# Optimization experiments

Measured on AMD Instinct MI355X. Metric: run time of the kernel, lower is better.

## Reference

```python
import jax, jax.numpy as jnp
import numpy as np

B, L, D = 4, 512, 128

def setup_inputs() -> dict:
    key = jax.random.key(0)
    k1, k2, k3, k4 = jax.random.split(key, 4)
    s = 1.0 / np.sqrt(D)
    return {
        "inp": jax.random.normal(k1, (B, L, D), dtype=jnp.float32),
        "Wu": jax.random.normal(k2, (D, D), dtype=jnp.float32) * s,
        "Ww": jax.random.normal(k3, (D, D), dtype=jnp.float32) * s,
        "Wv": jax.random.normal(k4, (1, D), dtype=jnp.float32) * s,
    }

def reference(inp, Wu, Ww, Wv):
    # inp: (B,L,D); torch Linear weights are (out,in), so y = x @ W.T
    qu = inp @ Wu.T                      # (B,L,D), u(inp)
    kw = inp @ Ww.T                      # (B,L,D), w(inp)
    # qu.unsqueeze(1) -> broadcast over i; kw.unsqueeze(2) -> broadcast over j
    # h[b,i,j,:] = tanh(u(inp)[b,j] + w(inp)[b,i])   (dropout = identity in eval)
    h = jnp.tanh(qu[:, None, :, :] + kw[:, :, None, :])   # (B,L,L,D)
    score = jnp.einsum('bijd,d->bij', h, Wv[0])           # (B,L,L)
    attn = jax.nn.softmax(score, axis=2)                  # softmax over keys j
    out = jnp.einsum('bij,bjd->bid', attn, inp)           # bmm(attn, inp)
    return out, attn
```

## Files before the change

### kernel.cpp

```cpp
#include <hip/hip_runtime.h>

#define BD 128
#define SL 512
#define NB 4

__device__ __forceinline__ float rcp_fast(float x) { return __builtin_amdgcn_rcpf(x); }

__global__ __launch_bounds__(256) void k_tr(const float* __restrict__ Wu,
                                            const float* __restrict__ Ww,
                                            float* __restrict__ WuT,
                                            float* __restrict__ WwT) {
    int idx = blockIdx.x * 256 + threadIdx.x;
    int k = idx >> 7, o = idx & 127;
    WuT[idx] = Wu[o * BD + k];
    WwT[idx] = Ww[o * BD + k];
}

__global__ __launch_bounds__(256) void k_qk(const float* __restrict__ inp,
                                            const float* __restrict__ WuT,
                                            const float* __restrict__ WwT,
                                            float* __restrict__ Equ2,
                                            float* __restrict__ Ekw) {
    __shared__ float sx[2][BD];
    const int t = threadIdx.x, m = t >> 7, o = t & 127;
    const int blk = blockIdx.x;
    const int x   = blk & 7;
    const int b   = x >> 1;
    const int rp  = (blk >> 3) * 2 + (x & 1);
    const int r0  = b * SL + rp * 2;
    const int l0  = rp * 2;
    const int jp  = l0 >> 1;

    sx[t >> 7][t & 127] = inp[(size_t)r0 * BD + t];
    __syncthreads();

    const float* WT = m ? WwT : WuT;
    float acc0 = 0.f, acc1 = 0.f;
    #pragma unroll 4
    for (int k = 0; k < BD; k += 4) {
        float w0 = WT[(k + 0) * BD + o];
        float w1 = WT[(k + 1) * BD + o];
        float w2 = WT[(k + 2) * BD + o];
        float w3 = WT[(k + 3) * BD + o];
        float4 x0 = *(const float4*)&sx[0][k];
        float4 x1 = *(const float4*)&sx[1][k];
        acc0 = fmaf(x0.x, w0, acc0); acc0 = fmaf(x0.y, w1, acc0);
        acc0 = fmaf(x0.z, w2, acc0); acc0 = fmaf(x0.w, w3, acc0);
        acc1 = fmaf(x1.x, w0, acc1); acc1 = fmaf(x1.y, w1, acc1);
        acc1 = fmaf(x1.z, w2, acc1); acc1 = fmaf(x1.w, w3, acc1);
    }

    if (m == 0) {
        size_t base = (((size_t)b * 32 + (o >> 2)) * 256 + jp) * 8 + (o & 3);
        Equ2[base]     = __expf(2.f * acc0);
        Equ2[base + 4] = __expf(2.f * acc1);
    } else {
        Ekw[(size_t)(r0 + 0) * BD + o] = __expf(2.f * acc0);
        Ekw[(size_t)(r0 + 1) * BD + o] = __expf(2.f * acc1);
    }
}

__global__ __launch_bounds__(1024, 8) void k_attn(const float* __restrict__ inp,
                                                  const float* __restrict__ Wv,
                                                  const float* __restrict__ Equ2,
                                                  const float* __restrict__ Ekw,
                                                  float* __restrict__ out,
                                                  float* __restrict__ attn) {
    __shared__ float  s_pT[SL * 4];
    __shared__ float  s_ap[8192];
    __shared__ float4 s_E[BD];
    __shared__ float  s_u[BD];
    __shared__ float  s_rB[4 * 8];

    const int t   = threadIdx.x;
    const int blk = blockIdx.x;
    const int x   = blk & 7;
    const int b   = x >> 1;
    const int it  = (blk >> 3) * 2 + (x & 1);
    const int i0  = it * 4;

    if (t < BD) {
        const float* ek = Ekw + ((size_t)b * SL + i0) * BD + t;
        float u = rcp_fast(Wv[t]);
        s_E[t] = make_float4(ek[0] * u, ek[BD] * u, ek[2 * BD] * u, ek[3 * BD] * u);
        s_u[t] = u;
    }
    __syncthreads();

    const int jp = t & 255, dg = t >> 8;
    const float4* equ4 = (const float4*)(Equ2 + (size_t)b * BD * SL);
    float a0[4] = {0.f, 0.f, 0.f, 0.f};
    float a1[4] = {0.f, 0.f, 0.f, 0.f};
    #pragma unroll 2
    for (int cc = 0; cc < 8; ++cc) {
        int c = dg * 8 + cc;
        float4 qA = equ4[(c * 256 + jp) * 2 + 0];
        float4 qB = equ4[(c * 256 + jp) * 2 + 1];
        float4 E0 = s_E[c * 4 + 0];
        float4 E1 = s_E[c * 4 + 1];
        float4 E2 = s_E[c * 4 + 2];
        float4 E3 = s_E[c * 4 + 3];
        float4 uu = *(const float4*)&s_u[c * 4];
        float e0[4] = {E0.x, E0.y, E0.z, E0.w};
        float e1[4] = {E1.x, E1.y, E1.z, E1.w};
        float e2[4] = {E2.x, E2.y, E2.z, E2.w};
        float e3[4] = {E3.x, E3.y, E3.z, E3.w};
        #pragma unroll
        for (int i = 0; i < 4; ++i) {
            float xa0 = fmaf(qA.x, e0[i], uu.x);
            float xa1 = fmaf(qA.y, e1[i], uu.y);
            a0[i] = fmaf(xa0 + xa1, rcp_fast(xa0 * xa1), a0[i]);
            float xa2 = fmaf(qA.z, e2[i], uu.z);
            float xa3 = fmaf(qA.w, e3[i], uu.w);
            a0[i] = fmaf(xa2 + xa3, rcp_fast(xa2 * xa3), a0[i]);
            float xb0 = fmaf(qB.x, e0[i], uu.x);
            float xb1 = fmaf(qB.y, e1[i], uu.y);
            a1[i] = fmaf(xb0 + xb1, rcp_fast(xb0 * xb1), a1[i]);
            float xb2 = fmaf(qB.z, e2[i], uu.z);
            float xb3 = fmaf(qB.w, e3[i], uu.w);
            a1[i] = fmaf(xb2 + xb3, rcp_fast(xb2 * xb3), a1[i]);
        }
    }
    #pragma unroll
    for (int i = 0; i < 4; ++i) {
        s_ap[((dg * 2 + 0) * 4 + i) * 256 + jp] = a0[i];
        s_ap[((dg * 2 + 1) * 4 + i) * 256 + jp] = a1[i];
    }
    __syncthreads();

    const int j = t & 511, dh = t >> 9, ro = dh * 2;
    const int jpp = j >> 1, jj = j & 1, w8 = j >> 6;
    float af[2];
    #pragma unroll
    for (int ii = 0; ii < 2; ++ii) {
        int r = ro + ii;
        af[ii] = s_ap[((0 * 2 + jj) * 4 + r) * 256 + jpp]
               + s_ap[((1 * 2 + jj) * 4 + r) * 256 + jpp]
               + s_ap[((2 * 2 + jj) * 4 + r) * 256 + jpp]
               + s_ap[((3 * 2 + jj) * 4 + r) * 256 + jpp];
    }
    float p0 = __expf(-2.f * af[0]);
    float p1 = __expf(-2.f * af[1]);
    float sm0 = p0, sm1 = p1;
    #pragma unroll
    for (int off = 32; off > 0; off >>= 1) {
        sm0 += __shfl_xor(sm0, off, 64);
        sm1 += __shfl_xor(sm1, off, 64);
    }
    if ((j & 63) == 0) { s_rB[(ro + 0) * 8 + w8] = sm0; s_rB[(ro + 1) * 8 + w8] = sm1; }
    __syncthreads();
    float n0, n1;
    {
        float4 r0 = *(const float4*)&s_rB[(ro + 0) * 8];
        float4 r1 = *(const float4*)&s_rB[(ro + 0) * 8 + 4];
        n0 = p0 * rcp_fast((r0.x + r0.y) + (r0.z + r0.w) + (r1.x + r1.y) + (r1.z + r1.w));
        float4 s0 = *(const float4*)&s_rB[(ro + 1) * 8];
        float4 s1 = *(const float4*)&s_rB[(ro + 1) * 8 + 4];
        n1 = p1 * rcp_fast((s0.x + s0.y) + (s0.z + s0.w) + (s1.x + s1.y) + (s1.z + s1.w));
    }
    attn[((size_t)b * SL + i0 + ro + 0) * SL + j] = n0;
    attn[((size_t)b * SL + i0 + ro + 1) * SL + j] = n1;
    ((float2*)s_pT)[j * 2 + dh] = make_float2(n0, n1);
    __syncthreads();

    const int g  = t >> 6;
    const int ln = t & 63;
    const int dq = ln & 31;
    const int rh = ln >> 5;
    const float4* inp4 = (const float4*)(inp + (size_t)b * SL * BD);
    float4 acc0 = make_float4(0.f, 0.f, 0.f, 0.f);
    float4 acc1 = make_float4(0.f, 0.f, 0.f, 0.f);
    #pragma unroll 4
    for (int jjj = 0; jjj < 32; ++jjj) {
        int jr = g * 32 + jjj;
        float4 xv = inp4[jr * 32 + dq];
        float2 pp = ((const float2*)s_pT)[jr * 2 + rh];
        acc0.x = fmaf(pp.x, xv.x, acc0.x); acc0.y = fmaf(pp.x, xv.y, acc0.y);
        acc0.z = fmaf(pp.x, xv.z, acc0.z); acc0.w = fmaf(pp.x, xv.w, acc0.w);
        acc1.x = fmaf(pp.y, xv.x, acc1.x); acc1.y = fmaf(pp.y, xv.y, acc1.y);
        acc1.z = fmaf(pp.y, xv.z, acc1.z); acc1.w = fmaf(pp.y, xv.w, acc1.w);
    }
    float* s_fin = s_ap;
    *(float4*)&s_fin[((g * 4) + rh * 2 + 0) * BD + dq * 4] = acc0;
    *(float4*)&s_fin[((g * 4) + rh * 2 + 1) * BD + dq * 4] = acc1;
    __syncthreads();
    if (t < 512) {
        int row = t >> 7, d = t & 127;
        float s = 0.f;
        #pragma unroll
        for (int gg = 0; gg < 16; ++gg)
            s += s_fin[(gg * 4 + row) * BD + d];
        out[((size_t)b * SL + i0 + row) * BD + d] = s;
    }
}

extern "C" void kernel_launch(void* const* d_in, const int* in_sizes, int n_in,
                              void* d_out, int out_size, void* d_ws, size_t ws_size,
                              hipStream_t stream) {
    const float* inp = (const float*)d_in[0];
    const float* Wu  = (const float*)d_in[1];
    const float* Ww  = (const float*)d_in[2];
    const float* Wv  = (const float*)d_in[3];

    float* out  = (float*)d_out;
    float* attn = out + (size_t)NB * SL * BD;

    float* ws   = (float*)d_ws;
    float* Equ2 = ws;
    float* Ekw  = Equ2 + (size_t)NB * BD * SL;
    float* WuT  = Ekw + (size_t)NB * SL * BD;
    float* WwT  = WuT + BD * BD;

    k_tr  <<<BD * BD / 256, 256, 0, stream>>>(Wu, Ww, WuT, WwT);
    k_qk  <<<NB * SL / 2, 256, 0, stream>>>(inp, WuT, WwT, Equ2, Ekw);
    k_attn<<<NB * SL / 4, 1024, 0, stream>>>(inp, Wv, Equ2, Ekw, out, attn);
}
```

Measured before the change: 88.66 us.

## Combine four tanh terms per reciprocal and use one thread per key column

Rewrites the attention kernel so each of 512 threads owns one key column and all 4 query rows, looping over all 128 features. This removes the cross-thread partial-score reduction through shared memory. The score accumulation now merges four 1/x terms with a single reciprocal instead of two, which halves the rcp count but adds multiplies and raises overflow risk in the products. The Equ layout is changed to match, and the block size drops from 1024 to 512 threads, giving each thread more work in the output matmul.

```diff
diff --git a/kernel.cpp b/kernel.cpp
--- a/kernel.cpp
+++ b/kernel.cpp
@@ -19,7 +19,7 @@
 __global__ __launch_bounds__(256) void k_qk(const float* __restrict__ inp,
                                             const float* __restrict__ WuT,
                                             const float* __restrict__ WwT,
-                                            float* __restrict__ Equ2,
+                                            float* __restrict__ Equ,
                                             float* __restrict__ Ekw) {
     __shared__ float sx[2][BD];
     const int t = threadIdx.x, m = t >> 7, o = t & 127;
@@ -29,7 +29,6 @@
     const int rp  = (blk >> 3) * 2 + (x & 1);
     const int r0  = b * SL + rp * 2;
     const int l0  = rp * 2;
-    const int jp  = l0 >> 1;
 
     sx[t >> 7][t & 127] = inp[(size_t)r0 * BD + t];
     __syncthreads();
@@ -51,144 +50,130 @@
     }
 
     if (m == 0) {
-        size_t base = (((size_t)b * 32 + (o >> 2)) * 256 + jp) * 8 + (o & 3);
-        Equ2[base]     = __expf(2.f * acc0);
-        Equ2[base + 4] = __expf(2.f * acc1);
+        size_t base = ((size_t)b * 32 + (o >> 2)) * (SL * 4) + (size_t)l0 * 4 + (o & 3);
+        Equ[base]     = __expf(2.f * acc0);
+        Equ[base + 4] = __expf(2.f * acc1);
     } else {
         Ekw[(size_t)(r0 + 0) * BD + o] = __expf(2.f * acc0);
         Ekw[(size_t)(r0 + 1) * BD + o] = __expf(2.f * acc1);
     }
 }
 
-__global__ __launch_bounds__(1024, 8) void k_attn(const float* __restrict__ inp,
-                                                  const float* __restrict__ Wv,
-                                                  const float* __restrict__ Equ2,
-                                                  const float* __restrict__ Ekw,
-                                                  float* __restrict__ out,
-                                                  float* __restrict__ attn) {
-    __shared__ float  s_pT[SL * 4];
-    __shared__ float  s_ap[8192];
-    __shared__ float4 s_E[BD];
-    __shared__ float  s_u[BD];
-    __shared__ float  s_rB[4 * 8];
-
-    const int t   = threadIdx.x;
+__device__ __forceinline__ void quad_acc(const float4 q, const float4 u4,
+                                         const float4 e, float& acc) {
+    float x0 = fmaf(q.x, e.x, u4.x);
+    float x1 = fmaf(q.y, e.y, u4.y);
+    float x2 = fmaf(q.z, e.z, u4.z);
+    float x3 = fmaf(q.w, e.w, u4.w);
+    float p01 = x0 * x1, p23 = x2 * x3;
+    float num = fmaf(x0 + x1, p23, (x2 + x3) * p01);
+    acc = fmaf(num, rcp_fast(p01 * p23), acc);
+}
+
+__global__ __launch_bounds__(512, 4) void k_attn(const float* __restrict__ inp,
+                                                 const float* __restrict__ Wv,
+                                                 const float* __restrict__ Equ,
+                                                 const float* __restrict__ Ekw,
+                                                 float* __restrict__ out,
+                                                 float* __restrict__ attn) {
+    __shared__ float4 s_E2[32][4];
+    __shared__ float4 s_u4[32];
+    __shared__ float4 s_pT[SL];
+    __shared__ float  s_fin[32 * BD];
+    __shared__ float4 s_red[8];
+
+    const int j   = threadIdx.x;
     const int blk = blockIdx.x;
     const int x   = blk & 7;
     const int b   = x >> 1;
     const int it  = (blk >> 3) * 2 + (x & 1);
     const int i0  = it * 4;
 
-    if (t < BD) {
-        const float* ek = Ekw + ((size_t)b * SL + i0) * BD + t;
-        float u = rcp_fast(Wv[t]);
-        s_E[t] = make_float4(ek[0] * u, ek[BD] * u, ek[2 * BD] * u, ek[3 * BD] * u);
-        s_u[t] = u;
-    }
-    __syncthreads();
-
-    const int jp = t & 255, dg = t >> 8;
-    const float4* equ4 = (const float4*)(Equ2 + (size_t)b * BD * SL);
-    float a0[4] = {0.f, 0.f, 0.f, 0.f};
-    float a1[4] = {0.f, 0.f, 0.f, 0.f};
-    #pragma unroll 2
-    for (int cc = 0; cc < 8; ++cc) {
-        int c = dg * 8 + cc;
-        float4 qA = equ4[(c * 256 + jp) * 2 + 0];
-        float4 qB = equ4[(c * 256 + jp) * 2 + 1];
-        float4 E0 = s_E[c * 4 + 0];
-        float4 E1 = s_E[c * 4 + 1];
-        float4 E2 = s_E[c * 4 + 2];
-        float4 E3 = s_E[c * 4 + 3];
-        float4 uu = *(const float4*)&s_u[c * 4];
-        float e0[4] = {E0.x, E0.y, E0.z, E0.w};
-        float e1[4] = {E1.x, E1.y, E1.z, E1.w};
-        float e2[4] = {E2.x, E2.y, E2.z, E2.w};
-        float e3[4] = {E3.x, E3.y, E3.z, E3.w};
-        #pragma unroll
-        for (int i = 0; i < 4; ++i) {
-            float xa0 = fmaf(qA.x, e0[i], uu.x);
-            float xa1 = fmaf(qA.y, e1[i], uu.y);
-            a0[i] = fmaf(xa0 + xa1, rcp_fast(xa0 * xa1), a0[i]);
-            float xa2 = fmaf(qA.z, e2[i], uu.z);
-            float xa3 = fmaf(qA.w, e3[i], uu.w);
-            a0[i] = fmaf(xa2 + xa3, rcp_fast(xa2 * xa3), a0[i]);
-            float xb0 = fmaf(qB.x, e0[i], uu.x);
-            float xb1 = fmaf(qB.y, e1[i], uu.y);
-            a1[i] = fmaf(xb0 + xb1, rcp_fast(xb0 * xb1), a1[i]);
-            float xb2 = fmaf(qB.z, e2[i], uu.z);
-            float xb3 = fmaf(qB.w, e3[i], uu.w);
-            a1[i] = fmaf(xb2 + xb3, rcp_fast(xb2 * xb3), a1[i]);
-        }
-    }
-    #pragma unroll
-    for (int i = 0; i < 4; ++i) {
-        s_ap[((dg * 2 + 0) * 4 + i) * 256 + jp] = a0[i];
-        s_ap[((dg * 2 + 1) * 4 + i) * 256 + jp] = a1[i];
-    }
-    __syncthreads();
-
-    const int j = t & 511, dh = t >> 9, ro = dh * 2;
-    const int jpp = j >> 1, jj = j & 1, w8 = j >> 6;
-    float af[2];
-    #pragma unroll
-    for (int ii = 0; ii < 2; ++ii) {
-        int r = ro + ii;
-        af[ii] = s_ap[((0 * 2 + jj) * 4 + r) * 256 + jpp]
-               + s_ap[((1 * 2 + jj) * 4 + r) * 256 + jpp]
-               + s_ap[((2 * 2 + jj) * 4 + r) * 256 + jpp]
-               + s_ap[((3 * 2 + jj) * 4 + r) * 256 + jpp];
-    }
-    float p0 = __expf(-2.f * af[0]);
-    float p1 = __expf(-2.f * af[1]);
-    float sm0 = p0, sm1 = p1;
+    if (j < BD) {
+        const float* ek = Ekw + ((size_t)b * SL + i0) * BD + j;
+        float u = rcp_fast(Wv[j]);
+        int c = j >> 2, kk = j & 3;
+        ((float*)&s_E2[c][0])[kk] = ek[0]        * u;
+        ((float*)&s_E2[c][1])[kk] = ek[BD]       * u;
+        ((float*)&s_E2[c][2])[kk] = ek[2 * BD]   * u;
+        ((float*)&s_E2[c][3])[kk] = ek[3 * BD]   * u;
+        ((float*)&s_u4[c])[kk]    = u;
+    }
+    __syncthreads();
+
+    const float4* equ4 = (const float4*)(Equ) + (size_t)b * 32 * SL;
+    float a0 = 0.f, a1 = 0.f, a2 = 0.f, a3 = 0.f;
+    #pragma unroll 4
+    for (int c = 0; c < 32; ++c) {
+        float4 q  = equ4[c * SL + j];
+        float4 u4 = s_u4[c];
+        float4 e0 = s_E2[c][0];
+        float4 e1 = s_E2[c][1];
+        float4 e2 = s_E2[c][2];
+        float4 e3 = s_E2[c][3];
+        quad_acc(q, u4, e0, a0);
+        quad_acc(q, u4, e1, a1);
+        quad_acc(q, u4, e2, a2);
+        quad_acc(q, u4, e3, a3);
+    }
+
+    float p0 = __expf(-2.f * a0);
+    float p1 = __expf(-2.f * a1);
+    float p2 = __expf(-2.f * a2);
+    float p3 = __expf(-2.f * a3);
+    float r0 = p0, r1 = p1, r2 = p2, r3 = p3;
     #pragma unroll
     for (int off = 32; off > 0; off >>= 1) {
-        sm0 += __shfl_xor(sm0, off, 64);
-        sm1 += __shfl_xor(sm1, off, 64);
-    }
-    if ((j & 63) == 0) { s_rB[(ro + 0) * 8 + w8] = sm0; s_rB[(ro + 1) * 8 + w8] = sm1; }
-    __syncthreads();
-    float n0, n1;
+        r0 += __shfl_xor(r0, off, 64);
+        r1 += __shfl_xor(r1, off, 64);
+        r2 += __shfl_xor(r2, off, 64);
+        r3 += __shfl_xor(r3, off, 64);
+    }
+    const int w = j >> 6, ln = j & 63;
+    if (ln == 0) s_red[w] = make_float4(r0, r1, r2, r3);
+    __syncthreads();
+    float4 d0 = s_red[0], d1 = s_red[1], d2 = s_red[2], d3 = s_red[3];
+    float4 d4 = s_red[4], d5 = s_red[5], d6 = s_red[6], d7 = s_red[7];
+    float dx = ((d0.x + d1.x) + (d2.x + d3.x)) + ((d4.x + d5.x) + (d6.x + d7.x));
+    float dy = ((d0.y + d1.y) + (d2.y + d3.y)) + ((d4.y + d5.y) + (d6.y + d7.y));
+    float dz = ((d0.z + d1.z) + (d2.z + d3.z)) + ((d4.z + d5.z) + (d6.z + d7.z));
+    float dw = ((d0.w + d1.w) + (d2.w + d3.w)) + ((d4.w + d5.w) + (d6.w + d7.w));
+    float n0 = p0 * rcp_fast(dx);
+    float n1 = p1 * rcp_fast(dy);
+    float n2 = p2 * rcp_fast(dz);
+    float n3 = p3 * rcp_fast(dw);
+    float* ap = attn + ((size_t)b * SL + i0) * SL + j;
+    ap[0]      = n0;
+    ap[SL]     = n1;
+    ap[2 * SL] = n2;
+    ap[3 * SL] = n3;
+    s_pT[j] = make_float4(n0, n1, n2, n3);
+    __syncthreads();
+
+    const int g  = j >> 6;
+    const int dq = j & 31;
+    const int rh = (j >> 5) & 1;
+    const float4* inp4 = (const float4*)(inp) + (size_t)b * SL * 32;
+    float4 accA = make_float4(0.f, 0.f, 0.f, 0.f);
+    float4 accB = make_float4(0.f, 0.f, 0.f, 0.f);
+    #pragma unroll 4
+    for (int tt = 0; tt < 64; ++tt) {
+        int jr = g * 64 + tt;
+        float4 xv = inp4[jr * 32 + dq];
+        float2 pp = *((const float2*)&s_pT[jr] + rh);
+        accA.x = fmaf(pp.x, xv.x, accA.x); accA.y = fmaf(pp.x, xv.y, accA.y);
+        accA.z = fmaf(pp.x, xv.z, accA.z); accA.w = fmaf(pp.x, xv.w, accA.w);
+        accB.x = fmaf(pp.y, xv.x, accB.x); accB.y = fmaf(pp.y, xv.y, accB.y);
+        accB.z = fmaf(pp.y, xv.z, accB.z); accB.w = fmaf(pp.y, xv.w, accB.w);
+    }
+    *(float4*)&s_fin[((g * 4) + rh * 2 + 0) * BD + dq * 4] = accA;
+    *(float4*)&s_fin[((g * 4) + rh * 2 + 1) * BD + dq * 4] = accB;
+    __syncthreads();
     {
-        float4 r0 = *(const float4*)&s_rB[(ro + 0) * 8];
-        float4 r1 = *(const float4*)&s_rB[(ro + 0) * 8 + 4];
-        n0 = p0 * rcp_fast((r0.x + r0.y) + (r0.z + r0.w) + (r1.x + r1.y) + (r1.z + r1.w));
-        float4 s0 = *(const float4*)&s_rB[(ro + 1) * 8];
-        float4 s1 = *(const float4*)&s_rB[(ro + 1) * 8 + 4];
-        n1 = p1 * rcp_fast((s0.x + s0.y) + (s0.z + s0.w) + (s1.x + s1.y) + (s1.z + s1.w));
-    }
-    attn[((size_t)b * SL + i0 + ro + 0) * SL + j] = n0;
-    attn[((size_t)b * SL + i0 + ro + 1) * SL + j] = n1;
-    ((float2*)s_pT)[j * 2 + dh] = make_float2(n0, n1);
-    __syncthreads();
-
-    const int g  = t >> 6;
-    const int ln = t & 63;
-    const int dq = ln & 31;
-    const int rh = ln >> 5;
-    const float4* inp4 = (const float4*)(inp + (size_t)b * SL * BD);
-    float4 acc0 = make_float4(0.f, 0.f, 0.f, 0.f);
-    float4 acc1 = make_float4(0.f, 0.f, 0.f, 0.f);
-    #pragma unroll 4
-    for (int jjj = 0; jjj < 32; ++jjj) {
-        int jr = g * 32 + jjj;
-        float4 xv = inp4[jr * 32 + dq];
-        float2 pp = ((const float2*)s_pT)[jr * 2 + rh];
-        acc0.x = fmaf(pp.x, xv.x, acc0.x); acc0.y = fmaf(pp.x, xv.y, acc0.y);
-        acc0.z = fmaf(pp.x, xv.z, acc0.z); acc0.w = fmaf(pp.x, xv.w, acc0.w);
-        acc1.x = fmaf(pp.y, xv.x, acc1.x); acc1.y = fmaf(pp.y, xv.y, acc1.y);
-        acc1.z = fmaf(pp.y, xv.z, acc1.z); acc1.w = fmaf(pp.y, xv.w, acc1.w);
-    }
-    float* s_fin = s_ap;
-    *(float4*)&s_fin[((g * 4) + rh * 2 + 0) * BD + dq * 4] = acc0;
-    *(float4*)&s_fin[((g * 4) + rh * 2 + 1) * BD + dq * 4] = acc1;
-    __syncthreads();
-    if (t < 512) {
-        int row = t >> 7, d = t & 127;
+        int row = j >> 7, d = j & 127;
         float s = 0.f;
         #pragma unroll
-        for (int gg = 0; gg < 16; ++gg)
+        for (int gg = 0; gg < 8; ++gg)
             s += s_fin[(gg * 4 + row) * BD + d];
         out[((size_t)b * SL + i0 + row) * BD + d] = s;
     }
@@ -206,12 +191,12 @@
     float* attn = out + (size_t)NB * SL * BD;
 
     float* ws   = (float*)d_ws;
-    float* Equ2 = ws;
-    float* Ekw  = Equ2 + (size_t)NB * BD * SL;
+    float* Equ  = ws;
+    float* Ekw  = Equ + (size_t)NB * BD * SL;
     float* WuT  = Ekw + (size_t)NB * SL * BD;
     float* WwT  = WuT + BD * BD;
 
     k_tr  <<<BD * BD / 256, 256, 0, stream>>>(Wu, Ww, WuT, WwT);
-    k_qk  <<<NB * SL / 2, 256, 0, stream>>>(inp, WuT, WwT, Equ2, Ekw);
-    k_attn<<<NB * SL / 4, 1024, 0, stream>>>(inp, Wv, Equ2, Ekw, out, attn);
-}
+    k_qk  <<<NB * SL / 2, 256, 0, stream>>>(inp, WuT, WwT, Equ, Ekw);
+    k_attn<<<NB * SL / 4, 512, 0, stream>>>(inp, Wv, Equ, Ekw, out, attn);
+}
```

New measurement: 89.77 us. About the same (+1.3%).
